# Kernel tuning notes

Hardware: AMD Instinct MI355X
Metric: run time of the kernel (lower is better)

The kernel has to match this reference:

```python
import jax, jax.numpy as jnp
import numpy as np

N_COMPANY = 16384
N_SECTOR = 64
PER_SECTOR = N_COMPANY // N_SECTOR  # 256, companies grouped contiguously by sector
WIN = 32
D_IN = 16
H_GRU = 64
H_INTRA = 64
H_INTER = 64
D_OUT = 4
E_INNER = 524288  # avg degree 32 within sectors


def setup_inputs() -> dict:
    key = jax.random.key(0)
    ks = jax.random.split(key, 20)
    s = 0.05

    daily_data_batch = jax.random.normal(ks[0], (WIN, N_COMPANY, D_IN), jnp.float32)

    rng = np.random.default_rng(0)
    dst = rng.integers(0, N_COMPANY, E_INNER)
    src = (dst // PER_SECTOR) * PER_SECTOR + rng.integers(0, PER_SECTOR, E_INNER)  # same-sector neighbors
    inner_edge = jnp.asarray(np.stack([src, dst]), jnp.int32)

    a, b = np.meshgrid(np.arange(N_SECTOR), np.arange(N_SECTOR), indexing="ij")
    oe = np.stack([a.ravel(), b.ravel()])
    oe = oe[:, oe[0] != oe[1]]  # fully-connected sector graph w/o self loops (GAT adds them)
    outer_edge = jnp.asarray(oe, jnp.int32)

    sector_ids = jnp.asarray(np.arange(N_COMPANY) // PER_SECTOR, jnp.int32)

    inp = {
        "daily_data_batch": daily_data_batch,
        "inner_edge": inner_edge,
        "outer_edge": outer_edge,
        "sector_ids": sector_ids,
        # BatchNorm1d(input_dim*window_size)
        "bn_gamma": jnp.ones((D_IN * WIN,), jnp.float32),
        "bn_beta": jnp.zeros((D_IN * WIN,), jnp.float32),
        # Graph GRU (per-node learnable initial hidden state)
        "gru_Wih": s * jax.random.normal(ks[1], (D_IN, 3 * H_GRU), jnp.float32),
        "gru_Whh": s * jax.random.normal(ks[2], (H_GRU, 3 * H_GRU), jnp.float32),
        "gru_bih": jnp.zeros((3 * H_GRU,), jnp.float32),
        "gru_bhh": jnp.zeros((3 * H_GRU,), jnp.float32),
        "gru_h0": s * jax.random.normal(ks[3], (N_COMPANY, H_GRU), jnp.float32),
        # intra-sector GATConv
        "gat1_W": s * jax.random.normal(ks[4], (H_GRU, H_INTRA), jnp.float32),
        "gat1_asrc": s * jax.random.normal(ks[5], (H_INTRA,), jnp.float32),
        "gat1_adst": s * jax.random.normal(ks[6], (H_INTRA,), jnp.float32),
        "gat1_b": jnp.zeros((H_INTRA,), jnp.float32),
        # inter-sector GATConv
        "gat2_W": s * jax.random.normal(ks[7], (H_INTRA, H_INTER), jnp.float32),
        "gat2_asrc": s * jax.random.normal(ks[8], (H_INTER,), jnp.float32),
        "gat2_adst": s * jax.random.normal(ks[9], (H_INTER,), jnp.float32),
        "gat2_b": jnp.zeros((H_INTER,), jnp.float32),
        # fusion / logit heads
        "fusion_W": s * jax.random.normal(ks[10], (H_GRU + H_INTRA + H_INTER, H_GRU), jnp.float32),
        "fusion_b": jnp.zeros((H_GRU,), jnp.float32),
        "logit_W": s * jax.random.normal(ks[11], (H_GRU, D_OUT), jnp.float32),
        "logit_b": jnp.zeros((D_OUT,), jnp.float32),
    }
    return inp


def _gat(x, edge, W, a_src, a_dst, b):
    """PyG-style single-head GATConv with default add_self_loops=True."""
    N = x.shape[0]
    h = x @ W  # [N, F]
    loops = jnp.arange(N, dtype=edge.dtype)
    src = jnp.concatenate([edge[0], loops])
    dst = jnp.concatenate([edge[1], loops])
    e = jax.nn.leaky_relu(h[src] @ a_src + h[dst] @ a_dst, 0.2)  # [E]
    # segment softmax over incoming edges per dst node
    m = jax.ops.segment_max(e, dst, num_segments=N)
    ex = jnp.exp(e - m[dst])
    denom = jax.ops.segment_sum(ex, dst, num_segments=N)
    alpha = ex / (denom[dst] + 1e-16)
    out = jax.ops.segment_sum(h[src] * alpha[:, None], dst, num_segments=N)
    return out + b


def _forward(daily_data_batch, inner_edge, outer_edge, sector_ids,
             bn_gamma, bn_beta,
             gru_Wih, gru_Whh, gru_bih, gru_bhh, gru_h0,
             gat1_W, gat1_asrc, gat1_adst, gat1_b,
             gat2_W, gat2_asrc, gat2_adst, gat2_b,
             fusion_W, fusion_b, logit_W, logit_b):
    W, N, D = daily_data_batch.shape
    # BatchNorm1d over companies (train-mode batch stats, eps=1e-5)
    xb = jnp.transpose(daily_data_batch, (1, 0, 2)).reshape(N, W * D)
    mu = xb.mean(axis=0)
    var = xb.var(axis=0)
    xb = (xb - mu) * jax.lax.rsqrt(var + 1e-5) * bn_gamma + bn_beta
    x = jnp.transpose(xb.reshape(N, W, D), (1, 0, 2))  # [W, N, D]

    # GRU over the window, per-node hidden state
    def step(h, xt):
        gi = xt @ gru_Wih + gru_bih
        gh = h @ gru_Whh + gru_bhh
        ir, iz, inn = jnp.split(gi, 3, axis=-1)
        hr, hz, hn = jnp.split(gh, 3, axis=-1)
        r = jax.nn.sigmoid(ir + hr)
        z = jax.nn.sigmoid(iz + hz)
        n = jnp.tanh(inn + r * hn)
        return (1.0 - z) * n + z * h, None

    seq_emb, _ = jax.lax.scan(step, gru_h0, x)  # [N, H_GRU]

    intra_emb = _gat(seq_emb, inner_edge, gat1_W, gat1_asrc, gat1_adst, gat1_b)  # [N, H_INTRA]

    # sector_separater + per-sector max pooling == segment_max
    sec_pool = jax.ops.segment_max(intra_emb, sector_ids, num_segments=N_SECTOR)  # [S, H_INTRA]
    sec_emb = _gat(sec_pool, outer_edge, gat2_W, gat2_asrc, gat2_adst, gat2_b)  # [S, H_INTER]
    sec_broad = sec_emb[sector_ids]  # repeat_interleave back to companies

    fusion_vec = jnp.concatenate([seq_emb, sec_broad, intra_emb], axis=-1)
    fusion_vec = jax.nn.relu(fusion_vec @ fusion_W + fusion_b)
    logits = jax.nn.softmax(fusion_vec @ logit_W + logit_b, axis=1)
    logits = jnp.cumsum(logits, axis=1)
    eps = 5e-08
    return jnp.clip(logits, eps, 1.0 - eps)


def reference(daily_data_batch, inner_edge, outer_edge, sector_ids,
              bn_gamma, bn_beta,
              gru_Wih, gru_Whh, gru_bih, gru_bhh, gru_h0,
              gat1_W, gat1_asrc, gat1_adst, gat1_b,
              gat2_W, gat2_asrc, gat2_adst, gat2_b,
              fusion_W, fusion_b, logit_W, logit_b):
    return _forward(daily_data_batch, inner_edge, outer_edge, sector_ids,
                    bn_gamma, bn_beta,
                    gru_Wih, gru_Whh, gru_bih, gru_bhh, gru_h0,
                    gat1_W, gat1_asrc, gat1_adst, gat1_b,
                    gat2_W, gat2_asrc, gat2_adst, gat2_b,
                    fusion_W, fusion_b, logit_W, logit_b)
```

## Files before the change

kernel.cpp:

```cpp
#include <hip/hip_runtime.h>

#define NC 16384
#define WIN 32
#define DI 16
#define EI 524288

typedef unsigned short u16;
typedef unsigned char u8;
typedef unsigned int u32;
typedef __attribute__((ext_vector_type(8))) short bfrag8;
typedef __attribute__((ext_vector_type(4))) float facc4;

__device__ __forceinline__ float bf2f(u16 u) { return __uint_as_float(((u32)u) << 16); }
__device__ __forceinline__ u16 f2bf(float f) {
    u32 u = __float_as_uint(f);
    u += 0x7FFFu + ((u >> 16) & 1u);
    return (u16)(u >> 16);
}
__device__ __forceinline__ float frcp(float x) { return __builtin_amdgcn_rcpf(x); }
__device__ __forceinline__ float ex2(float x) {
#if __has_builtin(__builtin_amdgcn_exp2f)
    return __builtin_amdgcn_exp2f(x);
#else
    return __expf(x * 0.69314718055994531f);
// ... 54 lines not shown
                                                 const void* __restrict__ fb,
                                                 const void* __restrict__ lw,
                                                 const void* __restrict__ lb,
                                                 float* __restrict__ ws,
                                                 uint4* __restrict__ M16) {
    int gt = blockIdx.x * 256 + threadIdx.x;
    const int GS = 64 * 256;
    bool f32 = is_f32(gamma);
    const float KR = -1.4426950408889634f;
    const float KN = -2.8853900817779268f;
    u16* fw16 = (u16*)(ws + O_FW16);
    for (int i = gt; i < 12288; i += GS)
        fw16[i] = f32 ? f2bf(((const float*)fw)[i]) : ((const u16*)fw)[i];
    for (int i = gt; i < 4096; i += GS) {
        ws[O_G1W + i] = loadf(g1w, i, f32);
        ws[O_G2W + i] = loadf(g2w, i, f32);
    }
    if (gt < 64) {
        ws[O_G1AS + gt] = loadf(g1as, gt, f32);
        ws[O_G1AD + gt] = loadf(g1ad, gt, f32);
        ws[O_G1B + gt] = loadf(g1b, gt, f32);
        ws[O_G2AS + gt] = loadf(g2as, gt, f32);
        ws[O_G2AD + gt] = loadf(g2ad, gt, f32);
        ws[O_G2B + gt] = loadf(g2b, gt, f32);
        ws[O_FB + gt] = loadf(fb, gt, f32);
    }
    if (gt < 256) ws[O_LW + gt] = loadf(lw, gt, f32);
    if (gt < 4) ws[O_LB + gt] = loadf(lb, gt, f32);
    for (int i = gt; i < 1024; i += GS) ws[O_BNACC + i] = 0.f;
    const uint4 z4 = {0u, 0u, 0u, 0u};
    for (int i = gt; i < 262144; i += GS) M16[i] = z4;

    for (int i = gt; i < 9216; i += GS) {
        int trow = i / 72;
        int idx = i % 72;
        int w_ = trow >> 6, lane_ = trow & 63, li_ = lane_ & 15, q_ = lane_ >> 4;
        u16 lo, hi;
        if (idx < 48) {
            int g = idx >> 4, rem = idx & 15;
            int ntl = rem >> 3, kc = (rem >> 2) & 1, j2 = rem & 3;
            float sc = (g < 2) ? KR : KN;
            int col = g * 64 + w_ * 32 + ntl * 16 + li_;
            int k = kc * 32 + q_ * 8 + j2 * 2;
            lo = f2bf(sc * loadf(whh, (size_t)k * 192 + col, f32));
            hi = f2bf(sc * loadf(whh, (size_t)(k + 1) * 192 + col, f32));
        } else {
            int idx2 = idx - 48;
            int g = idx2 >> 3, ntl = (idx2 >> 2) & 1, j2 = idx2 & 3;
            float sc = (g < 2) ? KR : KN;
            int col = g * 64 + w_ * 32 + ntl * 16 + li_;
            int k = q_ * 8 + j2 * 2;
            lo = (k < 16) ? f2bf(sc * loadf(wih, (size_t)k * 192 + col, f32)) : (u16)0;
            hi = (k + 1 < 16) ? f2bf(sc * loadf(wih, (size_t)(k + 1) * 192 + col, f32)) : (u16)0;
        }
        ((u32*)(ws + O_WIMG))[i] = (u32)lo | ((u32)hi << 16);
    }
    for (int i = gt; i < 1024; i += GS) {
        int trow = i >> 3, e = i & 7;
        int w_ = trow >> 6, lane_ = trow & 63, li_ = lane_ & 15;
        int ntl = e & 1, kind = e >> 1;
        int c = w_ * 32 + ntl * 16 + li_;
        float v;
        if (kind == 0) v = KR * (loadf(bih, c, f32) + loadf(bhh, c, f32));
        else if (kind == 1) v = KR * (loadf(bih, 64 + c, f32) + loadf(bhh, 64 + c, f32));
        else if (kind == 2) v = KN * loadf(bih, 128 + c, f32);
        else v = KN * loadf(bhh, 128 + c, f32);
        ws[O_BIMG + i] = v;
    }
}

__global__ __launch_bounds__(256) void k_prep(const void* __restrict__ daily,
                                              const void* __restrict__ gamma,
                                              float* __restrict__ bnacc,
                                              const int* __restrict__ edges,
                                              u32* __restrict__ M32) {
    __shared__ float rS[256 * 17];
    __shared__ float rQ[256 * 17];
    int bid = blockIdx.x;
    int tid = threadIdx.x;
    if (bid >= 128) {
        int g = (bid - 128) * 256 + tid;
        int4 s4 = ((const int4*)edges)[g];
        int4 d4 = ((const int4*)(edges + EI))[g];
        int ss[4] = {s4.x, s4.y, s4.z, s4.w};
        int dd[4] = {d4.x, d4.y, d4.z, d4.w};
#pragma unroll
        for (int i = 0; i < 4; i++) {
            int sl = ss[i] & 255;
            atomicAdd(&M32[dd[i] * 64 + (sl >> 2)], 1u << ((sl & 3) * 8));
        }
        return;
    }
    int w = bid >> 2, ch = bid & 3;
    bool f32 = is_f32(gamma);
    float s[16], q[16];
#pragma unroll
    for (int i = 0; i < 16; i++) { s[i] = 0.f; q[i] = 0.f; }
    for (int it = 0; it < 16; it++) {
        int c = ch * 4096 + it * 256 + tid;
        size_t base = ((size_t)w * NC + c) * DI;
        float v[16];
        if (f32) {
            const float4* p = (const float4*)((const float*)daily + base);
            float4 a = p[0], b = p[1], cc = p[2], d = p[3];
            v[0] = a.x; v[1] = a.y; v[2] = a.z; v[3] = a.w;
            v[4] = b.x; v[5] = b.y; v[6] = b.z; v[7] = b.w;
            v[8] = cc.x; v[9] = cc.y; v[10] = cc.z; v[11] = cc.w;
            v[12] = d.x; v[13] = d.y; v[14] = d.z; v[15] = d.w;
        } else {
            const uint4* p = (const uint4*)((const u16*)daily + base);
            uint4 a = p[0], b = p[1];
            u32 us[8] = {a.x, a.y, a.z, a.w, b.x, b.y, b.z, b.w};
#pragma unroll
            for (int i = 0; i < 8; i++) {
                v[2 * i] = __uint_as_float(us[i] << 16);
                v[2 * i + 1] = __uint_as_float(us[i] & 0xFFFF0000u);
            }
        }
#pragma unroll
        for (int i = 0; i < 16; i++) { s[i] += v[i]; q[i] += v[i] * v[i]; }
    }
#pragma unroll
    for (int i = 0; i < 16; i++) { rS[tid * 17 + i] = s[i]; rQ[tid * 17 + i] = q[i]; }
    __syncthreads();
    int f = tid & 15, g = tid >> 4;
    float ss = 0.f, qq = 0.f;
    for (int t = g * 16; t < g * 16 + 16; t++) { ss += rS[t * 17 + f]; qq += rQ[t * 17 + f]; }
    atomicAdd(&bnacc[w * 16 + f], ss);
    atomicAdd(&bnacc[512 + w * 16 + f], qq);
}

__global__ __launch_bounds__(128, 2) void k_gru(const void* __restrict__ daily,
                                                const void* __restrict__ gamma,
                                                const void* __restrict__ beta,
                                                const void* __restrict__ h0_g,
                                                const float* __restrict__ ws,
                                                float* __restrict__ seq_out,
                                                u16* __restrict__ h1_out,
                                                float* __restrict__ asg,
                                                float* __restrict__ adg) {
    __shared__ __attribute__((aligned(16))) u16 sHd[2][16 * 72];
    __shared__ __attribute__((aligned(16))) u16 sXall[512 * 24];
    __shared__ float sSc[512], sSh[512];
    __shared__ float sRed[2][2][16];
    int tid = threadIdx.x;
    int w = tid >> 6, lane = tid & 63;
    int li = lane & 15, q = lane >> 4;
    int n0 = blockIdx.x * 16;
    bool f32 = is_f32(gamma);

    for (int f = tid; f < 512; f += 128) {
        float mu = ws[O_BNACC + f] * (1.0f / NC);
        float var = ws[O_BNACC + 512 + f] * (1.0f / NC) - mu * mu;
        float sc = loadf(gamma, f, f32) * rsqrtf(var + 1e-5f);
        sSc[f] = sc;
        sSh[f] = loadf(beta, f, f32) - mu * sc;
    }
    __syncthreads();

    for (int R = tid; R < 512; R += 128) {
        int t = R >> 4, m = R & 15;
        size_t base = ((size_t)t * NC + n0 + m) * DI;
        float xv[16];
        if (f32) {
            const float4* p = (const float4*)((const float*)daily + base);
            float4 a = p[0], b = p[1], c = p[2], d = p[3];
            xv[0] = a.x; xv[1] = a.y; xv[2] = a.z; xv[3] = a.w;
            xv[4] = b.x; xv[5] = b.y; xv[6] = b.z; xv[7] = b.w;
            xv[8] = c.x; xv[9] = c.y; xv[10] = c.z; xv[11] = c.w;
            xv[12] = d.x; xv[13] = d.y; xv[14] = d.z; xv[15] = d.w;
        } else {
            const uint4* p = (const uint4*)((const u16*)daily + base);
            uint4 a = p[0], b = p[1];
            u32 us[8] = {a.x, a.y, a.z, a.w, b.x, b.y, b.z, b.w};
#pragma unroll
            for (int i = 0; i < 8; i++) {
                xv[2 * i] = __uint_as_float(us[i] << 16);
                xv[2 * i + 1] = __uint_as_float(us[i] & 0xFFFF0000u);
            }
        }
        u32 pxu[8];
#pragma unroll
        for (int i = 0; i < 16; i += 2)
            pxu[i >> 1] = pk2bf(xv[i] * sSc[t * 16 + i] + sSh[t * 16 + i],
                                xv[i + 1] * sSc[t * 16 + i + 1] + sSh[t * 16 + i + 1]);
        *(uint4*)&sXall[R * 24] = *(const uint4*)&pxu[0];
        *(uint4*)&sXall[R * 24 + 8] = *(const uint4*)&pxu[4];
    }

    bfrag8 bh[3][2][2];
    bfrag8 bx[3][2];
    {
        const bfrag8* wf = (const bfrag8*)((const char*)(ws + O_WIMG) + (size_t)tid * 288);
        int c_ = 0;
#pragma unroll
        for (int g = 0; g < 3; g++)
#pragma unroll
            for (int ntl = 0; ntl < 2; ntl++)
#pragma unroll
                for (int kc = 0; kc < 2; kc++) bh[g][ntl][kc] = wf[c_++];
#pragma unroll
        for (int g = 0; g < 3; g++)
#pragma unroll
            for (int ntl = 0; ntl < 2; ntl++) bx[g][ntl] = wf[c_++];
    }
    float bRv[2], bZv[2], bNXv[2], bNHv[2];
    {
        const float4* bimg = (const float4*)(ws + O_BIMG);
        float4 b0 = bimg[tid * 2], b1 = bimg[tid * 2 + 1];
        bRv[0] = b0.x; bRv[1] = b0.y; bZv[0] = b0.z; bZv[1] = b0.w;
        bNXv[0] = b1.x; bNXv[1] = b1.y; bNHv[0] = b1.z; bNHv[1] = b1.w;
    }

    float hC[2][4];
#pragma unroll
    for (int ntl = 0; ntl < 2; ntl++)
#pragma unroll
        for (int r = 0; r < 4; r++)
            hC[ntl][r] = loadf(h0_g, (size_t)(n0 + q * 4 + r) * 64 + w * 32 + ntl * 16 + li, f32);
    {
        int hr = tid >> 3, hc = (tid & 7) * 8;
        u32 hw[4];
#pragma unroll
        for (int i = 0; i < 8; i += 2)
            hw[i >> 1] = pk2bf(loadf(h0_g, (size_t)(n0 + hr) * 64 + hc + i, f32),
                               loadf(h0_g, (size_t)(n0 + hr) * 64 + hc + i + 1, f32));
        *(uint4*)&sHd[0][hr * 72 + hc] = *(const uint4*)&hw[0];
    }
    __syncthreads();

    bfrag8 ax = (bfrag8){0, 0, 0, 0, 0, 0, 0, 0};
    if (q < 2) ax = *(const bfrag8*)&sXall[li * 24 + q * 8];
    for (int t = 0; t < WIN; t++) {
        int p = t & 1;
        bfrag8 ah0 = *(const bfrag8*)&sHd[p][li * 72 + q * 8];
        bfrag8 ah1 = *(const bfrag8*)&sHd[p][li * 72 + 32 + q * 8];
        int tn = (t + 1) & (WIN - 1);
        bfrag8 axn = (bfrag8){0, 0, 0, 0, 0, 0, 0, 0};
        if (q < 2) axn = *(const bfrag8*)&sXall[(tn * 16 + li) * 24 + q * 8];
#pragma unroll
        for (int ntl = 0; ntl < 2; ntl++) {
            facc4 aR = __builtin_amdgcn_mfma_f32_16x16x32_bf16(ax, bx[0][ntl], (facc4){bRv[ntl], bRv[ntl], bRv[ntl], bRv[ntl]}, 0, 0, 0);
            facc4 aZ = __builtin_amdgcn_mfma_f32_16x16x32_bf16(ax, bx[1][ntl], (facc4){bZv[ntl], bZv[ntl], bZv[ntl], bZv[ntl]}, 0, 0, 0);
            facc4 aNX = __builtin_amdgcn_mfma_f32_16x16x32_bf16(ax, bx[2][ntl], (facc4){bNXv[ntl], bNXv[ntl], bNXv[ntl], bNXv[ntl]}, 0, 0, 0);
            facc4 aNH = __builtin_amdgcn_mfma_f32_16x16x32_bf16(ah0, bh[2][ntl][0], (facc4){bNHv[ntl], bNHv[ntl], bNHv[ntl], bNHv[ntl]}, 0, 0, 0);
            aR = __builtin_amdgcn_mfma_f32_16x16x32_bf16(ah0, bh[0][ntl][0], aR, 0, 0, 0);
            aZ = __builtin_amdgcn_mfma_f32_16x16x32_bf16(ah0, bh[1][ntl][0], aZ, 0, 0, 0);
            aNH = __builtin_amdgcn_mfma_f32_16x16x32_bf16(ah1, bh[2][ntl][1], aNH, 0, 0, 0);
            aR = __builtin_amdgcn_mfma_f32_16x16x32_bf16(ah1, bh[0][ntl][1], aR, 0, 0, 0);
            aZ = __builtin_amdgcn_mfma_f32_16x16x32_bf16(ah1, bh[1][ntl][1], aZ, 0, 0, 0);
#pragma unroll
            for (int r = 0; r < 4; r++) {
                float gr = frcp(1.0f + ex2(aR[r]));
                float gz = frcp(1.0f + ex2(aZ[r]));
                float narg = aNX[r] + gr * aNH[r];
                float gn = 2.0f * frcp(1.0f + ex2(narg)) - 1.0f;
                hC[ntl][r] = gn + gz * (hC[ntl][r] - gn);
            }
            int colw = w * 32 + ntl * 16 + li;
#pragma unroll
            for (int rp = 0; rp < 4; rp += 2) {
                u32 pk = pk2bf(hC[ntl][rp], hC[ntl][rp + 1]);
                sHd[p ^ 1][(q * 4 + rp) * 72 + colw] = (u16)pk;
                sHd[p ^ 1][(q * 4 + rp + 1) * 72 + colw] = (u16)(pk >> 16);
            }
        }
        __syncthreads();
        ax = axn;
    }

#pragma unroll
    for (int ntl = 0; ntl < 2; ntl++)
#pragma unroll
        for (int r = 0; r < 4; r++)
            seq_out[(size_t)(n0 + q * 4 + r) * 64 + w * 32 + ntl * 16 + li] = hC[ntl][r];

    bfrag8 a0 = *(const bfrag8*)&sHd[0][li * 72 + q * 8];
    bfrag8 a1 = *(const bfrag8*)&sHd[0][li * 72 + 32 + q * 8];
    const facc4 zf = {0.f, 0.f, 0.f, 0.f};
    float pAs[4] = {0.f, 0.f, 0.f, 0.f}, pAd[4] = {0.f, 0.f, 0.f, 0.f};
#pragma unroll
    for (int ntl = 0; ntl < 2; ntl++) {
        int colw = w * 32 + ntl * 16 + li;
        bfrag8 bg0, bg1;
#pragma unroll
        for (int j = 0; j < 8; j++) {
            bg0[j] = (short)f2bf(ws[O_G1W + (q * 8 + j) * 64 + colw]);
            bg1[j] = (short)f2bf(ws[O_G1W + (32 + q * 8 + j) * 64 + colw]);
        }
        facc4 acc = __builtin_amdgcn_mfma_f32_16x16x32_bf16(a0, bg0, zf, 0, 0, 0);
        acc = __builtin_amdgcn_mfma_f32_16x16x32_bf16(a1, bg1, acc, 0, 0, 0);
        float a1s_j = ws[O_G1AS + colw], a1d_j = ws[O_G1AD + colw];
#pragma unroll
        for (int r = 0; r < 4; r++) {
            h1_out[(size_t)(n0 + q * 4 + r) * 64 + colw] = f2bf(acc[r]);
            pAs[r] += acc[r] * a1s_j;
            pAd[r] += acc[r] * a1d_j;
        }
    }
#pragma unroll
    for (int o = 1; o < 16; o <<= 1)
#pragma unroll
        for (int r = 0; r < 4; r++) {
            pAs[r] += __shfl_xor(pAs[r], o);
            pAd[r] += __shfl_xor(pAd[r], o);
        }
    if (li == 0) {
#pragma unroll
        for (int r = 0; r < 4; r++) {
            sRed[0][w][q * 4 + r] = pAs[r];
            sRed[1][w][q * 4 + r] = pAd[r];
        }
    }
    __syncthreads();
    if (tid < 16) {
        asg[n0 + tid] = sRed[0][0][tid] + sRed[0][1][tid];
        adg[n0 + tid] = sRed[1][0][tid] + sRed[1][1][tid];
    }
}

__global__ __launch_bounds__(256) void k_gat1agg(const u16* __restrict__ h1g,
                                                 const float* __restrict__ ws,
                                                 const u8* __restrict__ M8,
                                                 const float* __restrict__ asg,
                                                 const float* __restrict__ adg,
                                                 u16* __restrict__ intra,
                                                 float* __restrict__ spool8) {
    __shared__ __attribute__((aligned(16))) u16 hT[64 * 264];
    __shared__ __attribute__((aligned(16))) u16 sP[32 * 264];
    __shared__ float sAs[256], sAd[32], sB[64], sRS[32];
    __shared__ float sRSp[8][32];
    __shared__ float wmax[4];
    int tid = threadIdx.x;
    int sector = blockIdx.x >> 3;
    int dstbase = sector * 256 + (blockIdx.x & 7) * 32;
    int sbase = sector * 256;
    {
#pragma unroll
        for (int p = 0; p < 8; p++) {
            int row = p * 32 + (tid >> 3);
            int c0 = (tid & 7) * 8;
            uint4 v = *(const uint4*)(h1g + (size_t)(sbase + row) * 64 + c0);
            u16 e[8];
            *(uint4*)e = v;
#pragma unroll
            for (int i = 0; i < 8; i++) hT[(c0 + i) * 264 + row] = e[i];
        }
    }
    sAs[tid] = asg[sbase + tid];
    if (tid < 32) sAd[tid] = adg[dstbase + tid];
// ... 253 lines not shown
extern "C" void kernel_launch(void* const* d_in, const int* in_sizes, int n_in,
                              void* d_out, int out_size, void* d_ws, size_t ws_size,
                              hipStream_t stream) {
    const void* daily = d_in[0];
    const int* inner = (const int*)d_in[1];
    const void* gamma = d_in[4];
    const void* beta = d_in[5];
    const void* wih = d_in[6];
    const void* whh = d_in[7];
    const void* bih = d_in[8];
    const void* bhh = d_in[9];
    const void* h0 = d_in[10];
    const void* g1w = d_in[11];
    const void* g1as = d_in[12];
    const void* g1ad = d_in[13];
    const void* g1b = d_in[14];
    const void* g2w = d_in[15];
    const void* g2as = d_in[16];
    const void* g2ad = d_in[17];
    const void* g2b = d_in[18];
    const void* fw = d_in[19];
    const void* fb = d_in[20];
    const void* lw = d_in[21];
    const void* lb = d_in[22];

    float* ws = (float*)d_ws;
    u16* h1g = (u16*)(ws + O_H1);
    u16* intra = (u16*)(ws + O_INTRA);
    u8* M8 = (u8*)(ws + O_M);

    k_convert<<<64, 256, 0, stream>>>(gamma, wih, whh, bih, bhh, g1w, g1as, g1ad, g1b,
                                      g2w, g2as, g2ad, g2b, fw, fb, lw, lb, ws, (uint4*)M8);
    k_prep<<<640, 256, 0, stream>>>(daily, gamma, ws + O_BNACC, inner, (u32*)M8);
    k_gru<<<1024, 128, 0, stream>>>(daily, gamma, beta, h0, ws, ws + O_SEQ, h1g, ws + O_AS, ws + O_AD);
    k_gat1agg<<<512, 256, 0, stream>>>(h1g, ws, M8, ws + O_AS, ws + O_AD, intra, ws + O_SPOOL);
    k_fusion<<<256, 256, 0, stream>>>(ws + O_SEQ, ws + O_SPOOL, intra, ws, gamma, d_out);
}
```

Before: 215.7 us.

## Stream GRU inputs from global memory per step instead of staging in LDS

The GRU kernel no longer preloads all 32 timesteps of normalized inputs into a 24KB shared buffer. Each lane now prefetches raw input two steps ahead into registers and applies the batch-norm scale/shift with bf16 packing one step ahead, double-buffered across an unrolled pair of steps. With the LDS footprint shrunk, the launch bounds are raised to four blocks per CU to increase occupancy. The cost is exposing global-load latency inside the sequential recurrence and more register pressure under the tighter occupancy bound.

Result: slower. 317.9 us (+47.4%).

```diff
diff --git a/kernel.cpp b/kernel.cpp
--- a/kernel.cpp
+++ b/kernel.cpp
@@ -208,7 +208,7 @@
     atomicAdd(&bnacc[512 + w * 16 + f], qq);
 }
 
-__global__ __launch_bounds__(128, 2) void k_gru(const void* __restrict__ daily,
+__global__ __launch_bounds__(128, 4) void k_gru(const void* __restrict__ daily,
                                                 const void* __restrict__ gamma,
                                                 const void* __restrict__ beta,
                                                 const void* __restrict__ h0_g,
@@ -218,14 +218,30 @@
                                                 float* __restrict__ asg,
                                                 float* __restrict__ adg) {
     __shared__ __attribute__((aligned(16))) u16 sHd[2][16 * 72];
-    __shared__ __attribute__((aligned(16))) u16 sXall[512 * 24];
-    __shared__ float sSc[512], sSh[512];
+    __shared__ __attribute__((aligned(16))) float sSc[512];
+    __shared__ __attribute__((aligned(16))) float sSh[512];
     __shared__ float sRed[2][2][16];
     int tid = threadIdx.x;
     int w = tid >> 6, lane = tid & 63;
     int li = lane & 15, q = lane >> 4;
     int n0 = blockIdx.x * 16;
     bool f32 = is_f32(gamma);
+    const bool xl = (q < 2);
+
+    uint4 xrA[2], xrB[2];
+    if (xl) {
+        size_t b0 = ((size_t)(n0 + li)) * DI + q * 8;
+        size_t b1 = ((size_t)NC + n0 + li) * DI + q * 8;
+        if (f32) {
+            const uint4* p0 = (const uint4*)((const float*)daily + b0);
+            const uint4* p1 = (const uint4*)((const float*)daily + b1);
+            xrA[0] = p0[0]; xrA[1] = p0[1];
+            xrB[0] = p1[0]; xrB[1] = p1[1];
+        } else {
+            xrA[0] = *(const uint4*)((const u16*)daily + b0);
+            xrB[0] = *(const uint4*)((const u16*)daily + b1);
+        }
+    }
 
     for (int f = tid; f < 512; f += 128) {
         float mu = ws[O_BNACC + f] * (1.0f / NC);
@@ -234,37 +250,6 @@
         sSc[f] = sc;
         sSh[f] = loadf(beta, f, f32) - mu * sc;
     }
-    __syncthreads();
-
-    for (int R = tid; R < 512; R += 128) {
-        int t = R >> 4, m = R & 15;
-        size_t base = ((size_t)t * NC + n0 + m) * DI;
-        float xv[16];
-        if (f32) {
-            const float4* p = (const float4*)((const float*)daily + base);
-            float4 a = p[0], b = p[1], c = p[2], d = p[3];
-            xv[0] = a.x; xv[1] = a.y; xv[2] = a.z; xv[3] = a.w;
-            xv[4] = b.x; xv[5] = b.y; xv[6] = b.z; xv[7] = b.w;
-            xv[8] = c.x; xv[9] = c.y; xv[10] = c.z; xv[11] = c.w;
-            xv[12] = d.x; xv[13] = d.y; xv[14] = d.z; xv[15] = d.w;
-        } else {
-            const uint4* p = (const uint4*)((const u16*)daily + base);
-            uint4 a = p[0], b = p[1];
-            u32 us[8] = {a.x, a.y, a.z, a.w, b.x, b.y, b.z, b.w};
-#pragma unroll
-            for (int i = 0; i < 8; i++) {
-                xv[2 * i] = __uint_as_float(us[i] << 16);
-                xv[2 * i + 1] = __uint_as_float(us[i] & 0xFFFF0000u);
-            }
-        }
-        u32 pxu[8];
-#pragma unroll
-        for (int i = 0; i < 16; i += 2)
-            pxu[i >> 1] = pk2bf(xv[i] * sSc[t * 16 + i] + sSh[t * 16 + i],
-                                xv[i + 1] * sSc[t * 16 + i + 1] + sSh[t * 16 + i + 1]);
-        *(uint4*)&sXall[R * 24] = *(const uint4*)&pxu[0];
-        *(uint4*)&sXall[R * 24 + 8] = *(const uint4*)&pxu[4];
-    }
 
     bfrag8 bh[3][2][2];
     bfrag8 bx[3][2];
@@ -307,45 +292,99 @@
     }
     __syncthreads();
 
+#define XCONV(TC, XSRC, AXOUT)                                                          \
+    {                                                                                   \
+        if (xl) {                                                                       \
+            float xv_[8];                                                               \
+            if (f32) {                                                                  \
+                *(uint4*)&xv_[0] = XSRC[0];                                             \
+                *(uint4*)&xv_[4] = XSRC[1];                                             \
+            } else {                                                                    \
+                u32 u0_ = XSRC[0].x, u1_ = XSRC[0].y, u2_ = XSRC[0].z, u3_ = XSRC[0].w; \
+                xv_[0] = __uint_as_float(u0_ << 16);                                    \
+                xv_[1] = __uint_as_float(u0_ & 0xFFFF0000u);                            \
+                xv_[2] = __uint_as_float(u1_ << 16);                                    \
+                xv_[3] = __uint_as_float(u1_ & 0xFFFF0000u);                            \
+                xv_[4] = __uint_as_float(u2_ << 16);                                    \
+                xv_[5] = __uint_as_float(u2_ & 0xFFFF0000u);                            \
+                xv_[6] = __uint_as_float(u3_ << 16);                                    \
+                xv_[7] = __uint_as_float(u3_ & 0xFFFF0000u);                            \
+            }                                                                           \
+            int cb_ = (TC) * 16 + q * 8;                                                \
+            float4 sA_ = *(const float4*)&sSc[cb_];                                     \
+            float4 sB_ = *(const float4*)&sSc[cb_ + 4];                                 \
+            float4 hA_ = *(const float4*)&sSh[cb_];                                     \
+            float4 hB_ = *(const float4*)&sSh[cb_ + 4];                                 \
+            union { u32 u[4]; bfrag8 f; } cv_;                                          \
+            cv_.u[0] = pk2bf(xv_[0] * sA_.x + hA_.x, xv_[1] * sA_.y + hA_.y);           \
+            cv_.u[1] = pk2bf(xv_[2] * sA_.z + hA_.z, xv_[3] * sA_.w + hA_.w);           \
+            cv_.u[2] = pk2bf(xv_[4] * sB_.x + hB_.x, xv_[5] * sB_.y + hB_.y);           \
+            cv_.u[3] = pk2bf(xv_[6] * sB_.z + hB_.z, xv_[7] * sB_.w + hB_.w);           \
+            AXOUT = cv_.f;                                                              \
+        }                                                                               \
+    }
+
+#define XLOAD(TL, XDST)                                                                 \
+    {                                                                                   \
+        if (xl) {                                                                       \
+            size_t base_ = ((size_t)(TL) * NC + n0 + li) * DI + q * 8;                  \
+            if (f32) {                                                                  \
+                const uint4* pp_ = (const uint4*)((const float*)daily + base_);         \
+                XDST[0] = pp_[0]; XDST[1] = pp_[1];                                     \
+            } else {                                                                    \
+                XDST[0] = *(const uint4*)((const u16*)daily + base_);                   \
+            }                                                                           \
+        }                                                                               \
+    }
+
+#define GRU_STEP(T, XDST, XSRC)                                                                                   \
+    {                                                                                                             \
+        const int p_ = (T) & 1;                                                                                   \
+        bfrag8 ah0 = *(const bfrag8*)&sHd[p_][li * 72 + q * 8];                                                   \
+        bfrag8 ah1 = *(const bfrag8*)&sHd[p_][li * 72 + 32 + q * 8];                                              \
+        XLOAD(((T) + 2) & 31, XDST);                                                                              \
+        bfrag8 axn = (bfrag8){0, 0, 0, 0, 0, 0, 0, 0};                                                            \
+        XCONV(((T) + 1) & 31, XSRC, axn);                                                                         \
+        _Pragma("unroll")                                                                                         \
+        for (int ntl = 0; ntl < 2; ntl++) {                                                                       \
+            facc4 aR = __builtin_amdgcn_mfma_f32_16x16x32_bf16(ax, bx[0][ntl], (facc4){bRv[ntl], bRv[ntl], bRv[ntl], bRv[ntl]}, 0, 0, 0); \
+            facc4 aZ = __builtin_amdgcn_mfma_f32_16x16x32_bf16(ax, bx[1][ntl], (facc4){bZv[ntl], bZv[ntl], bZv[ntl], bZv[ntl]}, 0, 0, 0); \
+            facc4 aNX = __builtin_amdgcn_mfma_f32_16x16x32_bf16(ax, bx[2][ntl], (facc4){bNXv[ntl], bNXv[ntl], bNXv[ntl], bNXv[ntl]}, 0, 0, 0); \
+            facc4 aNH = __builtin_amdgcn_mfma_f32_16x16x32_bf16(ah0, bh[2][ntl][0], (facc4){bNHv[ntl], bNHv[ntl], bNHv[ntl], bNHv[ntl]}, 0, 0, 0); \
+            aR = __builtin_amdgcn_mfma_f32_16x16x32_bf16(ah0, bh[0][ntl][0], aR, 0, 0, 0);                        \
+            aZ = __builtin_amdgcn_mfma_f32_16x16x32_bf16(ah0, bh[1][ntl][0], aZ, 0, 0, 0);                        \
+            aNH = __builtin_amdgcn_mfma_f32_16x16x32_bf16(ah1, bh[2][ntl][1], aNH, 0, 0, 0);                      \
+            aR = __builtin_amdgcn_mfma_f32_16x16x32_bf16(ah1, bh[0][ntl][1], aR, 0, 0, 0);                        \
+            aZ = __builtin_amdgcn_mfma_f32_16x16x32_bf16(ah1, bh[1][ntl][1], aZ, 0, 0, 0);                        \
+            _Pragma("unroll")                                                                                     \
+            for (int r = 0; r < 4; r++) {                                                                         \
+                float gr = frcp(1.0f + ex2(aR[r]));                                                               \
+                float gz = frcp(1.0f + ex2(aZ[r]));                                                               \
+                float narg = aNX[r] + gr * aNH[r];                                                                \
+                float gn = 2.0f * frcp(1.0f + ex2(narg)) - 1.0f;                                                  \
+                hC[ntl][r] = gn + gz * (hC[ntl][r] - gn);                                                         \
+            }                                                                                                     \
+            int colw = w * 32 + ntl * 16 + li;                                                                    \
+            _Pragma("unroll")                                                                                     \
+            for (int rp = 0; rp < 4; rp += 2) {                                                                   \
+                u32 pk = pk2bf(hC[ntl][rp], hC[ntl][rp + 1]);                                                     \
+                sHd[p_ ^ 1][(q * 4 + rp) * 72 + colw] = (u16)pk;                                                  \
+                sHd[p_ ^ 1][(q * 4 + rp + 1) * 72 + colw] = (u16)(pk >> 16);                                      \
+            }                                                                                                     \
+        }                                                                                                         \
+        __syncthreads();                                                                                          \
+        ax = axn;                                                                                                 \
+    }
+
     bfrag8 ax = (bfrag8){0, 0, 0, 0, 0, 0, 0, 0};
-    if (q < 2) ax = *(const bfrag8*)&sXall[li * 24 + q * 8];
-    for (int t = 0; t < WIN; t++) {
-        int p = t & 1;
-        bfrag8 ah0 = *(const bfrag8*)&sHd[p][li * 72 + q * 8];
-        bfrag8 ah1 = *(const bfrag8*)&sHd[p][li * 72 + 32 + q * 8];
-        int tn = (t + 1) & (WIN - 1);
-        bfrag8 axn = (bfrag8){0, 0, 0, 0, 0, 0, 0, 0};
-        if (q < 2) axn = *(const bfrag8*)&sXall[(tn * 16 + li) * 24 + q * 8];
-#pragma unroll
-        for (int ntl = 0; ntl < 2; ntl++) {
-            facc4 aR = __builtin_amdgcn_mfma_f32_16x16x32_bf16(ax, bx[0][ntl], (facc4){bRv[ntl], bRv[ntl], bRv[ntl], bRv[ntl]}, 0, 0, 0);
-            facc4 aZ = __builtin_amdgcn_mfma_f32_16x16x32_bf16(ax, bx[1][ntl], (facc4){bZv[ntl], bZv[ntl], bZv[ntl], bZv[ntl]}, 0, 0, 0);
-            facc4 aNX = __builtin_amdgcn_mfma_f32_16x16x32_bf16(ax, bx[2][ntl], (facc4){bNXv[ntl], bNXv[ntl], bNXv[ntl], bNXv[ntl]}, 0, 0, 0);
-            facc4 aNH = __builtin_amdgcn_mfma_f32_16x16x32_bf16(ah0, bh[2][ntl][0], (facc4){bNHv[ntl], bNHv[ntl], bNHv[ntl], bNHv[ntl]}, 0, 0, 0);
-            aR = __builtin_amdgcn_mfma_f32_16x16x32_bf16(ah0, bh[0][ntl][0], aR, 0, 0, 0);
-            aZ = __builtin_amdgcn_mfma_f32_16x16x32_bf16(ah0, bh[1][ntl][0], aZ, 0, 0, 0);
-            aNH = __builtin_amdgcn_mfma_f32_16x16x32_bf16(ah1, bh[2][ntl][1], aNH, 0, 0, 0);
-            aR = __builtin_amdgcn_mfma_f32_16x16x32_bf16(ah1, bh[0][ntl][1], aR, 0, 0, 0);
-            aZ = __builtin_amdgcn_mfma_f32_16x16x32_bf16(ah1, bh[1][ntl][1], aZ, 0, 0, 0);
-#pragma unroll
-            for (int r = 0; r < 4; r++) {
-                float gr = frcp(1.0f + ex2(aR[r]));
-                float gz = frcp(1.0f + ex2(aZ[r]));
-                float narg = aNX[r] + gr * aNH[r];
-                float gn = 2.0f * frcp(1.0f + ex2(narg)) - 1.0f;
-                hC[ntl][r] = gn + gz * (hC[ntl][r] - gn);
-            }
-            int colw = w * 32 + ntl * 16 + li;
-#pragma unroll
-            for (int rp = 0; rp < 4; rp += 2) {
-                u32 pk = pk2bf(hC[ntl][rp], hC[ntl][rp + 1]);
-                sHd[p ^ 1][(q * 4 + rp) * 72 + colw] = (u16)pk;
-                sHd[p ^ 1][(q * 4 + rp + 1) * 72 + colw] = (u16)(pk >> 16);
-            }
-        }
-        __syncthreads();
-        ax = axn;
-    }
+    XCONV(0, xrA, ax);
+    for (int t2 = 0; t2 < WIN; t2 += 2) {
+        GRU_STEP(t2, xrA, xrB);
+        GRU_STEP(t2 + 1, xrB, xrA);
+    }
+#undef GRU_STEP
+#undef XLOAD
+#undef XCONV
 
 #pragma unroll
     for (int ntl = 0; ntl < 2; ntl++)
```

## Stream GRU inputs from global per timestep instead of staging all in LDS

Applied to the files above, without the earlier changes.

Removes the upfront staging of all 32 timesteps of normalized input into a 24KB shared buffer. Each step now prefetches the next timestep's raw input into registers and applies batchnorm and bf16 packing just before the barrier, overlapping the global load with the MFMA work. The cut in LDS use allows higher occupancy, so the min-blocks launch bound hint is dropped. The cost is global load latency inside the serial recurrence and more register pressure.

Result: slower. 221.8 us (+2.8%).

```diff
diff --git a/kernel.cpp b/kernel.cpp
--- a/kernel.cpp
+++ b/kernel.cpp
@@ -208,24 +208,36 @@
     atomicAdd(&bnacc[512 + w * 16 + f], qq);
 }
 
-__global__ __launch_bounds__(128, 2) void k_gru(const void* __restrict__ daily,
-                                                const void* __restrict__ gamma,
-                                                const void* __restrict__ beta,
-                                                const void* __restrict__ h0_g,
-                                                const float* __restrict__ ws,
-                                                float* __restrict__ seq_out,
-                                                u16* __restrict__ h1_out,
-                                                float* __restrict__ asg,
-                                                float* __restrict__ adg) {
+__global__ __launch_bounds__(128) void k_gru(const void* __restrict__ daily,
+                                             const void* __restrict__ gamma,
+                                             const void* __restrict__ beta,
+                                             const void* __restrict__ h0_g,
+                                             const float* __restrict__ ws,
+                                             float* __restrict__ seq_out,
+                                             u16* __restrict__ h1_out,
+                                             float* __restrict__ asg,
+                                             float* __restrict__ adg) {
     __shared__ __attribute__((aligned(16))) u16 sHd[2][16 * 72];
-    __shared__ __attribute__((aligned(16))) u16 sXall[512 * 24];
-    __shared__ float sSc[512], sSh[512];
+    __shared__ __attribute__((aligned(16))) float sSc[512];
+    __shared__ __attribute__((aligned(16))) float sSh[512];
     __shared__ float sRed[2][2][16];
     int tid = threadIdx.x;
     int w = tid >> 6, lane = tid & 63;
     int li = lane & 15, q = lane >> 4;
     int n0 = blockIdx.x * 16;
     bool f32 = is_f32(gamma);
+    const bool xl = (q < 2);
+
+    uint4 xr[2];
+    if (xl) {
+        size_t b0 = ((size_t)(n0 + li)) * DI + q * 8;
+        if (f32) {
+            const uint4* p0 = (const uint4*)((const float*)daily + b0);
+            xr[0] = p0[0]; xr[1] = p0[1];
+        } else {
+            xr[0] = *(const uint4*)((const u16*)daily + b0);
+        }
+    }
 
     for (int f = tid; f < 512; f += 128) {
         float mu = ws[O_BNACC + f] * (1.0f / NC);
@@ -234,37 +246,6 @@
         sSc[f] = sc;
         sSh[f] = loadf(beta, f, f32) - mu * sc;
     }
-    __syncthreads();
-
-    for (int R = tid; R < 512; R += 128) {
-        int t = R >> 4, m = R & 15;
-        size_t base = ((size_t)t * NC + n0 + m) * DI;
-        float xv[16];
-        if (f32) {
-            const float4* p = (const float4*)((const float*)daily + base);
-            float4 a = p[0], b = p[1], c = p[2], d = p[3];
-            xv[0] = a.x; xv[1] = a.y; xv[2] = a.z; xv[3] = a.w;
-            xv[4] = b.x; xv[5] = b.y; xv[6] = b.z; xv[7] = b.w;
-            xv[8] = c.x; xv[9] = c.y; xv[10] = c.z; xv[11] = c.w;
-            xv[12] = d.x; xv[13] = d.y; xv[14] = d.z; xv[15] = d.w;
-        } else {
-            const uint4* p = (const uint4*)((const u16*)daily + base);
-            uint4 a = p[0], b = p[1];
-            u32 us[8] = {a.x, a.y, a.z, a.w, b.x, b.y, b.z, b.w};
-#pragma unroll
-            for (int i = 0; i < 8; i++) {
-                xv[2 * i] = __uint_as_float(us[i] << 16);
-                xv[2 * i + 1] = __uint_as_float(us[i] & 0xFFFF0000u);
-            }
-        }
-        u32 pxu[8];
-#pragma unroll
-        for (int i = 0; i < 16; i += 2)
-            pxu[i >> 1] = pk2bf(xv[i] * sSc[t * 16 + i] + sSh[t * 16 + i],
-                                xv[i + 1] * sSc[t * 16 + i + 1] + sSh[t * 16 + i + 1]);
-        *(uint4*)&sXall[R * 24] = *(const uint4*)&pxu[0];
-        *(uint4*)&sXall[R * 24 + 8] = *(const uint4*)&pxu[4];
-    }
 
     bfrag8 bh[3][2][2];
     bfrag8 bx[3][2];
@@ -307,15 +288,58 @@
     }
     __syncthreads();
 
+#define XCONV(TC, AXOUT)                                                              \
+    {                                                                                 \
+        if (xl) {                                                                     \
+            float xv_[8];                                                             \
+            if (f32) {                                                                \
+                *(uint4*)&xv_[0] = xr[0];                                             \
+                *(uint4*)&xv_[4] = xr[1];                                             \
+            } else {                                                                  \
+                u32 u0_ = xr[0].x, u1_ = xr[0].y, u2_ = xr[0].z, u3_ = xr[0].w;       \
+                xv_[0] = __uint_as_float(u0_ << 16);                                  \
+                xv_[1] = __uint_as_float(u0_ & 0xFFFF0000u);                          \
+                xv_[2] = __uint_as_float(u1_ << 16);                                  \
+                xv_[3] = __uint_as_float(u1_ & 0xFFFF0000u);                          \
+                xv_[4] = __uint_as_float(u2_ << 16);                                  \
+                xv_[5] = __uint_as_float(u2_ & 0xFFFF0000u);                          \
+                xv_[6] = __uint_as_float(u3_ << 16);                                  \
+                xv_[7] = __uint_as_float(u3_ & 0xFFFF0000u);                          \
+            }                                                                         \
+            int cb_ = (TC) * 16 + q * 8;                                              \
+            float4 sA_ = *(const float4*)&sSc[cb_];                                   \
+            float4 sB_ = *(const float4*)&sSc[cb_ + 4];                               \
+            float4 hA_ = *(const float4*)&sSh[cb_];                                   \
+            float4 hB_ = *(const float4*)&sSh[cb_ + 4];                               \
+            union { u32 u[4]; bfrag8 f; } cv_;                                        \
+            cv_.u[0] = pk2bf(xv_[0] * sA_.x + hA_.x, xv_[1] * sA_.y + hA_.y);         \
+            cv_.u[1] = pk2bf(xv_[2] * sA_.z + hA_.z, xv_[3] * sA_.w + hA_.w);         \
+            cv_.u[2] = pk2bf(xv_[4] * sB_.x + hB_.x, xv_[5] * sB_.y + hB_.y);         \
+            cv_.u[3] = pk2bf(xv_[6] * sB_.z + hB_.z, xv_[7] * sB_.w + hB_.w);         \
+            AXOUT = cv_.f;                                                            \
+        }                                                                             \
+    }
+
+#define XLOAD(TL)                                                                     \
+    {                                                                                 \
+        if (xl) {                                                                     \
+            size_t base_ = ((size_t)(TL) * NC + n0 + li) * DI + q * 8;                \
+            if (f32) {                                                                \
+                const uint4* pp_ = (const uint4*)((const float*)daily + base_);       \
+                xr[0] = pp_[0]; xr[1] = pp_[1];                                       \
+            } else {                                                                  \
+                xr[0] = *(const uint4*)((const u16*)daily + base_);                   \
+            }                                                                         \
+        }                                                                             \
+    }
+
     bfrag8 ax = (bfrag8){0, 0, 0, 0, 0, 0, 0, 0};
-    if (q < 2) ax = *(const bfrag8*)&sXall[li * 24 + q * 8];
+    XCONV(0, ax);
     for (int t = 0; t < WIN; t++) {
         int p = t & 1;
         bfrag8 ah0 = *(const bfrag8*)&sHd[p][li * 72 + q * 8];
         bfrag8 ah1 = *(const bfrag8*)&sHd[p][li * 72 + 32 + q * 8];
-        int tn = (t + 1) & (WIN - 1);
-        bfrag8 axn = (bfrag8){0, 0, 0, 0, 0, 0, 0, 0};
-        if (q < 2) axn = *(const bfrag8*)&sXall[(tn * 16 + li) * 24 + q * 8];
+        XLOAD((t + 1) & 31);
 #pragma unroll
         for (int ntl = 0; ntl < 2; ntl++) {
             facc4 aR = __builtin_amdgcn_mfma_f32_16x16x32_bf16(ax, bx[0][ntl], (facc4){bRv[ntl], bRv[ntl], bRv[ntl], bRv[ntl]}, 0, 0, 0);
@@ -343,9 +367,13 @@
                 sHd[p ^ 1][(q * 4 + rp + 1) * 72 + colw] = (u16)(pk >> 16);
             }
         }
+        bfrag8 axn = (bfrag8){0, 0, 0, 0, 0, 0, 0, 0};
+        XCONV((t + 1) & 31, axn);
         __syncthreads();
         ax = axn;
     }
+#undef XLOAD
+#undef XCONV
 
 #pragma unroll
     for (int ntl = 0; ntl < 2; ntl++)
```

## Split GRU hidden columns across four waves instead of two per block

Applied to the files above, without the earlier changes.

The GRU kernel now runs 256 threads (4 waves) per 16-node block, with each wave owning 16 hidden columns instead of 32. This halves the serial MFMA and gate work per wave in each of the 32 recurrent timesteps and shortens the dependent chain per step. The weight and bias images are re-laid out in the convert kernel to match, and the final attention reduction sums four partials. The trade-off is more waves contending at each per-step barrier, plus higher register and occupancy pressure per block.

New measurement: 212.7 us. About the same (-1.4%).

```diff
diff --git a/kernel.cpp b/kernel.cpp
--- a/kernel.cpp
+++ b/kernel.cpp
@@ -110,23 +110,22 @@
     for (int i = gt; i < 262144; i += GS) M16[i] = z4;
 
     for (int i = gt; i < 9216; i += GS) {
-        int trow = i / 72;
-        int idx = i % 72;
+        int trow = i / 36;
+        int idx = i % 36;
         int w_ = trow >> 6, lane_ = trow & 63, li_ = lane_ & 15, q_ = lane_ >> 4;
         u16 lo, hi;
-        if (idx < 48) {
-            int g = idx >> 4, rem = idx & 15;
-            int ntl = rem >> 3, kc = (rem >> 2) & 1, j2 = rem & 3;
+        if (idx < 24) {
+            int g = idx >> 3, kc = (idx >> 2) & 1, j2 = idx & 3;
             float sc = (g < 2) ? KR : KN;
-            int col = g * 64 + w_ * 32 + ntl * 16 + li_;
+            int col = g * 64 + w_ * 16 + li_;
             int k = kc * 32 + q_ * 8 + j2 * 2;
             lo = f2bf(sc * loadf(whh, (size_t)k * 192 + col, f32));
             hi = f2bf(sc * loadf(whh, (size_t)(k + 1) * 192 + col, f32));
         } else {
-            int idx2 = idx - 48;
-            int g = idx2 >> 3, ntl = (idx2 >> 2) & 1, j2 = idx2 & 3;
+            int idx2 = idx - 24;
+            int g = idx2 >> 2, j2 = idx2 & 3;
             float sc = (g < 2) ? KR : KN;
-            int col = g * 64 + w_ * 32 + ntl * 16 + li_;
+            int col = g * 64 + w_ * 16 + li_;
             int k = q_ * 8 + j2 * 2;
             lo = (k < 16) ? f2bf(sc * loadf(wih, (size_t)k * 192 + col, f32)) : (u16)0;
             hi = (k + 1 < 16) ? f2bf(sc * loadf(wih, (size_t)(k + 1) * 192 + col, f32)) : (u16)0;
@@ -134,14 +133,13 @@
         ((u32*)(ws + O_WIMG))[i] = (u32)lo | ((u32)hi << 16);
     }
     for (int i = gt; i < 1024; i += GS) {
-        int trow = i >> 3, e = i & 7;
+        int trow = i >> 2, e = i & 3;
         int w_ = trow >> 6, lane_ = trow & 63, li_ = lane_ & 15;
-        int ntl = e & 1, kind = e >> 1;
-        int c = w_ * 32 + ntl * 16 + li_;
+        int c = w_ * 16 + li_;
         float v;
-        if (kind == 0) v = KR * (loadf(bih, c, f32) + loadf(bhh, c, f32));
-        else if (kind == 1) v = KR * (loadf(bih, 64 + c, f32) + loadf(bhh, 64 + c, f32));
-        else if (kind == 2) v = KN * loadf(bih, 128 + c, f32);
+        if (e == 0) v = KR * (loadf(bih, c, f32) + loadf(bhh, c, f32));
+        else if (e == 1) v = KR * (loadf(bih, 64 + c, f32) + loadf(bhh, 64 + c, f32));
+        else if (e == 2) v = KN * loadf(bih, 128 + c, f32);
         else v = KN * loadf(bhh, 128 + c, f32);
         ws[O_BIMG + i] = v;
     }
@@ -208,26 +206,27 @@
     atomicAdd(&bnacc[512 + w * 16 + f], qq);
 }
 
-__global__ __launch_bounds__(128, 2) void k_gru(const void* __restrict__ daily,
-                                                const void* __restrict__ gamma,
-                                                const void* __restrict__ beta,
-                                                const void* __restrict__ h0_g,
-                                                const float* __restrict__ ws,
-                                                float* __restrict__ seq_out,
-                                                u16* __restrict__ h1_out,
-                                                float* __restrict__ asg,
-                                                float* __restrict__ adg) {
+__global__ __launch_bounds__(256) void k_gru(const void* __restrict__ daily,
+                                             const void* __restrict__ gamma,
+                                             const void* __restrict__ beta,
+                                             const void* __restrict__ h0_g,
+                                             const float* __restrict__ ws,
+                                             float* __restrict__ seq_out,
+                                             u16* __restrict__ h1_out,
+                                             float* __restrict__ asg,
+                                             float* __restrict__ adg) {
     __shared__ __attribute__((aligned(16))) u16 sHd[2][16 * 72];
     __shared__ __attribute__((aligned(16))) u16 sXall[512 * 24];
     __shared__ float sSc[512], sSh[512];
-    __shared__ float sRed[2][2][16];
+    __shared__ float sRed[2][4][16];
     int tid = threadIdx.x;
     int w = tid >> 6, lane = tid & 63;
     int li = lane & 15, q = lane >> 4;
     int n0 = blockIdx.x * 16;
+    int colw = w * 16 + li;
     bool f32 = is_f32(gamma);
 
-    for (int f = tid; f < 512; f += 128) {
+    for (int f = tid; f < 512; f += 256) {
         float mu = ws[O_BNACC + f] * (1.0f / NC);
         float var = ws[O_BNACC + 512 + f] * (1.0f / NC) - mu * mu;
         float sc = loadf(gamma, f, f32) * rsqrtf(var + 1e-5f);
@@ -236,7 +235,7 @@
     }
     __syncthreads();
 
-    for (int R = tid; R < 512; R += 128) {
+    for (int R = tid; R < 512; R += 256) {
         int t = R >> 4, m = R & 15;
         size_t base = ((size_t)t * NC + n0 + m) * DI;
         float xv[16];
@@ -266,44 +265,36 @@
         *(uint4*)&sXall[R * 24 + 8] = *(const uint4*)&pxu[4];
     }
 
-    bfrag8 bh[3][2][2];
-    bfrag8 bx[3][2];
-    {
-        const bfrag8* wf = (const bfrag8*)((const char*)(ws + O_WIMG) + (size_t)tid * 288);
+    bfrag8 bh[3][2];
+    bfrag8 bx[3];
+    {
+        const bfrag8* wf = (const bfrag8*)((const char*)(ws + O_WIMG) + (size_t)tid * 144);
         int c_ = 0;
 #pragma unroll
         for (int g = 0; g < 3; g++)
 #pragma unroll
-            for (int ntl = 0; ntl < 2; ntl++)
-#pragma unroll
-                for (int kc = 0; kc < 2; kc++) bh[g][ntl][kc] = wf[c_++];
-#pragma unroll
-        for (int g = 0; g < 3; g++)
-#pragma unroll
-            for (int ntl = 0; ntl < 2; ntl++) bx[g][ntl] = wf[c_++];
-    }
-    float bRv[2], bZv[2], bNXv[2], bNHv[2];
-    {
-        const float4* bimg = (const float4*)(ws + O_BIMG);
-        float4 b0 = bimg[tid * 2], b1 = bimg[tid * 2 + 1];
-        bRv[0] = b0.x; bRv[1] = b0.y; bZv[0] = b0.z; bZv[1] = b0.w;
-        bNXv[0] = b1.x; bNXv[1] = b1.y; bNHv[0] = b1.z; bNHv[1] = b1.w;
-    }
-
-    float hC[2][4];
-#pragma unroll
-    for (int ntl = 0; ntl < 2; ntl++)
-#pragma unroll
-        for (int r = 0; r < 4; r++)
-            hC[ntl][r] = loadf(h0_g, (size_t)(n0 + q * 4 + r) * 64 + w * 32 + ntl * 16 + li, f32);
-    {
-        int hr = tid >> 3, hc = (tid & 7) * 8;
-        u32 hw[4];
-#pragma unroll
-        for (int i = 0; i < 8; i += 2)
-            hw[i >> 1] = pk2bf(loadf(h0_g, (size_t)(n0 + hr) * 64 + hc + i, f32),
-                               loadf(h0_g, (size_t)(n0 + hr) * 64 + hc + i + 1, f32));
-        *(uint4*)&sHd[0][hr * 72 + hc] = *(const uint4*)&hw[0];
+            for (int kc = 0; kc < 2; kc++) bh[g][kc] = wf[c_++];
+#pragma unroll
+        for (int g = 0; g < 3; g++) bx[g] = wf[c_++];
+    }
+    float bR, bZ, bNX, bNH;
+    {
+        float4 b0 = ((const float4*)(ws + O_BIMG))[tid];
+        bR = b0.x; bZ = b0.y; bNX = b0.z; bNH = b0.w;
+    }
+
+    float hC[4];
+#pragma unroll
+    for (int r = 0; r < 4; r++)
+        hC[r] = loadf(h0_g, (size_t)(n0 + q * 4 + r) * 64 + colw, f32);
+    {
+        int hr = tid >> 4, hc = (tid & 15) * 4;
+        u32 a = pk2bf(loadf(h0_g, (size_t)(n0 + hr) * 64 + hc, f32),
+                      loadf(h0_g, (size_t)(n0 + hr) * 64 + hc + 1, f32));
+        u32 b = pk2bf(loadf(h0_g, (size_t)(n0 + hr) * 64 + hc + 2, f32),
+                      loadf(h0_g, (size_t)(n0 + hr) * 64 + hc + 3, f32));
+        uint2 v2; v2.x = a; v2.y = b;
+        *(uint2*)&sHd[0][hr * 72 + hc] = v2;
     }
     __syncthreads();
 
@@ -316,65 +307,55 @@
         int tn = (t + 1) & (WIN - 1);
         bfrag8 axn = (bfrag8){0, 0, 0, 0, 0, 0, 0, 0};
         if (q < 2) axn = *(const bfrag8*)&sXall[(tn * 16 + li) * 24 + q * 8];
-#pragma unroll
-        for (int ntl = 0; ntl < 2; ntl++) {
-            facc4 aR = __builtin_amdgcn_mfma_f32_16x16x32_bf16(ax, bx[0][ntl], (facc4){bRv[ntl], bRv[ntl], bRv[ntl], bRv[ntl]}, 0, 0, 0);
-            facc4 aZ = __builtin_amdgcn_mfma_f32_16x16x32_bf16(ax, bx[1][ntl], (facc4){bZv[ntl], bZv[ntl], bZv[ntl], bZv[ntl]}, 0, 0, 0);
-            facc4 aNX = __builtin_amdgcn_mfma_f32_16x16x32_bf16(ax, bx[2][ntl], (facc4){bNXv[ntl], bNXv[ntl], bNXv[ntl], bNXv[ntl]}, 0, 0, 0);
-            facc4 aNH = __builtin_amdgcn_mfma_f32_16x16x32_bf16(ah0, bh[2][ntl][0], (facc4){bNHv[ntl], bNHv[ntl], bNHv[ntl], bNHv[ntl]}, 0, 0, 0);
-            aR = __builtin_amdgcn_mfma_f32_16x16x32_bf16(ah0, bh[0][ntl][0], aR, 0, 0, 0);
-            aZ = __builtin_amdgcn_mfma_f32_16x16x32_bf16(ah0, bh[1][ntl][0], aZ, 0, 0, 0);
-            aNH = __builtin_amdgcn_mfma_f32_16x16x32_bf16(ah1, bh[2][ntl][1], aNH, 0, 0, 0);
-            aR = __builtin_amdgcn_mfma_f32_16x16x32_bf16(ah1, bh[0][ntl][1], aR, 0, 0, 0);
-            aZ = __builtin_amdgcn_mfma_f32_16x16x32_bf16(ah1, bh[1][ntl][1], aZ, 0, 0, 0);
-#pragma unroll
-            for (int r = 0; r < 4; r++) {
-                float gr = frcp(1.0f + ex2(aR[r]));
-                float gz = frcp(1.0f + ex2(aZ[r]));
-                float narg = aNX[r] + gr * aNH[r];
-                float gn = 2.0f * frcp(1.0f + ex2(narg)) - 1.0f;
-                hC[ntl][r] = gn + gz * (hC[ntl][r] - gn);
-            }
-            int colw = w * 32 + ntl * 16 + li;
-#pragma unroll
-            for (int rp = 0; rp < 4; rp += 2) {
-                u32 pk = pk2bf(hC[ntl][rp], hC[ntl][rp + 1]);
-                sHd[p ^ 1][(q * 4 + rp) * 72 + colw] = (u16)pk;
-                sHd[p ^ 1][(q * 4 + rp + 1) * 72 + colw] = (u16)(pk >> 16);
-            }
+        facc4 aR = __builtin_amdgcn_mfma_f32_16x16x32_bf16(ax, bx[0], (facc4){bR, bR, bR, bR}, 0, 0, 0);
+        facc4 aZ = __builtin_amdgcn_mfma_f32_16x16x32_bf16(ax, bx[1], (facc4){bZ, bZ, bZ, bZ}, 0, 0, 0);
+        facc4 aNX = __builtin_amdgcn_mfma_f32_16x16x32_bf16(ax, bx[2], (facc4){bNX, bNX, bNX, bNX}, 0, 0, 0);
+        facc4 aNH = __builtin_amdgcn_mfma_f32_16x16x32_bf16(ah0, bh[2][0], (facc4){bNH, bNH, bNH, bNH}, 0, 0, 0);
+        aR = __builtin_amdgcn_mfma_f32_16x16x32_bf16(ah0, bh[0][0], aR, 0, 0, 0);
+        aZ = __builtin_amdgcn_mfma_f32_16x16x32_bf16(ah0, bh[1][0], aZ, 0, 0, 0);
+        aNH = __builtin_amdgcn_mfma_f32_16x16x32_bf16(ah1, bh[2][1], aNH, 0, 0, 0);
+        aR = __builtin_amdgcn_mfma_f32_16x16x32_bf16(ah1, bh[0][1], aR, 0, 0, 0);
+        aZ = __builtin_amdgcn_mfma_f32_16x16x32_bf16(ah1, bh[1][1], aZ, 0, 0, 0);
+#pragma unroll
+        for (int r = 0; r < 4; r++) {
+            float gr = frcp(1.0f + ex2(aR[r]));
+            float gz = frcp(1.0f + ex2(aZ[r]));
+            float narg = aNX[r] + gr * aNH[r];
+            float gn = 2.0f * frcp(1.0f + ex2(narg)) - 1.0f;
+            hC[r] = gn + gz * (hC[r] - gn);
+        }
+#pragma unroll
+        for (int rp = 0; rp < 4; rp += 2) {
+            u32 pk = pk2bf(hC[rp], hC[rp + 1]);
+            sHd[p ^ 1][(q * 4 + rp) * 72 + colw] = (u16)pk;
+            sHd[p ^ 1][(q * 4 + rp + 1) * 72 + colw] = (u16)(pk >> 16);
         }
         __syncthreads();
         ax = axn;
     }
 
 #pragma unroll
-    for (int ntl = 0; ntl < 2; ntl++)
-#pragma unroll
-        for (int r = 0; r < 4; r++)
-            seq_out[(size_t)(n0 + q * 4 + r) * 64 + w * 32 + ntl * 16 + li] = hC[ntl][r];
+    for (int r = 0; r < 4; r++)
+        seq_out[(size_t)(n0 + q * 4 + r) * 64 + colw] = hC[r];
 
     bfrag8 a0 = *(const bfrag8*)&sHd[0][li * 72 + q * 8];
     bfrag8 a1 = *(const bfrag8*)&sHd[0][li * 72 + 32 + q * 8];
     const facc4 zf = {0.f, 0.f, 0.f, 0.f};
-    float pAs[4] = {0.f, 0.f, 0.f, 0.f}, pAd[4] = {0.f, 0.f, 0.f, 0.f};
-#pragma unroll
-    for (int ntl = 0; ntl < 2; ntl++) {
-        int colw = w * 32 + ntl * 16 + li;
-        bfrag8 bg0, bg1;
-#pragma unroll
-        for (int j = 0; j < 8; j++) {
-            bg0[j] = (short)f2bf(ws[O_G1W + (q * 8 + j) * 64 + colw]);
-            bg1[j] = (short)f2bf(ws[O_G1W + (32 + q * 8 + j) * 64 + colw]);
-        }
-        facc4 acc = __builtin_amdgcn_mfma_f32_16x16x32_bf16(a0, bg0, zf, 0, 0, 0);
-        acc = __builtin_amdgcn_mfma_f32_16x16x32_bf16(a1, bg1, acc, 0, 0, 0);
-        float a1s_j = ws[O_G1AS + colw], a1d_j = ws[O_G1AD + colw];
-#pragma unroll
-        for (int r = 0; r < 4; r++) {
-            h1_out[(size_t)(n0 + q * 4 + r) * 64 + colw] = f2bf(acc[r]);
-            pAs[r] += acc[r] * a1s_j;
-            pAd[r] += acc[r] * a1d_j;
-        }
+    bfrag8 bg0, bg1;
+#pragma unroll
+    for (int j = 0; j < 8; j++) {
+        bg0[j] = (short)f2bf(ws[O_G1W + (q * 8 + j) * 64 + colw]);
+        bg1[j] = (short)f2bf(ws[O_G1W + (32 + q * 8 + j) * 64 + colw]);
+    }
+    facc4 acc = __builtin_amdgcn_mfma_f32_16x16x32_bf16(a0, bg0, zf, 0, 0, 0);
+    acc = __builtin_amdgcn_mfma_f32_16x16x32_bf16(a1, bg1, acc, 0, 0, 0);
+    float a1s_j = ws[O_G1AS + colw], a1d_j = ws[O_G1AD + colw];
+    float pAs[4], pAd[4];
+#pragma unroll
+    for (int r = 0; r < 4; r++) {
+        h1_out[(size_t)(n0 + q * 4 + r) * 64 + colw] = f2bf(acc[r]);
+        pAs[r] = acc[r] * a1s_j;
+        pAd[r] = acc[r] * a1d_j;
     }
 #pragma unroll
     for (int o = 1; o < 16; o <<= 1)
@@ -392,8 +373,8 @@
     }
     __syncthreads();
     if (tid < 16) {
-        asg[n0 + tid] = sRed[0][0][tid] + sRed[0][1][tid];
-        adg[n0 + tid] = sRed[1][0][tid] + sRed[1][1][tid];
+        asg[n0 + tid] = sRed[0][0][tid] + sRed[0][1][tid] + sRed[0][2][tid] + sRed[0][3][tid];
+        adg[n0 + tid] = sRed[1][0][tid] + sRed[1][1][tid] + sRed[1][2][tid] + sRed[1][3][tid];
     }
 }
 
@@ -713,7 +694,7 @@
     k_convert<<<64, 256, 0, stream>>>(gamma, wih, whh, bih, bhh, g1w, g1as, g1ad, g1b,
                                       g2w, g2as, g2ad, g2b, fw, fb, lw, lb, ws, (uint4*)M8);
     k_prep<<<640, 256, 0, stream>>>(daily, gamma, ws + O_BNACC, inner, (u32*)M8);
-    k_gru<<<1024, 128, 0, stream>>>(daily, gamma, beta, h0, ws, ws + O_SEQ, h1g, ws + O_AS, ws + O_AD);
+    k_gru<<<1024, 256, 0, stream>>>(daily, gamma, beta, h0, ws, ws + O_SEQ, h1g, ws + O_AS, ws + O_AD);
     k_gat1agg<<<512, 256, 0, stream>>>(h1g, ws, M8, ws + O_AS, ws + O_AD, intra, ws + O_SPOOL);
     k_fusion<<<256, 256, 0, stream>>>(ws + O_SEQ, ws + O_SPOOL, intra, ws, gamma, d_out);
 }
```
